# Optimization experiments

Hardware: AMD Instinct MI355X
Metric: run time of the kernel (lower is better)

The kernel has to match this reference:

```python
import jax, jax.numpy as jnp
import numpy as np

N_NODES = 50000
D = 100          # hidden_size == out_size
STEP = 1
B, N, L = 512, 64, 64
STDV = 1.0 / np.sqrt(D)


def _uniform(key, shape):
    return jax.random.uniform(key, shape, jnp.float32, -STDV, STDV)


def setup_inputs() -> dict:
    key = jax.random.key(0)
    ks = jax.random.split(key, 16)
    inp = {
        'adj_in': jax.random.uniform(ks[0], (B, N, N), jnp.float32),
        'adj_out': jax.random.uniform(ks[1], (B, N, N), jnp.float32),
        'item': jax.random.randint(ks[2], (B, N), 0, N_NODES, jnp.int32),
        'alias': jax.random.randint(ks[3], (B, L), 0, N, jnp.int32),
        'mask': jnp.ones((B, L), jnp.float32),
        'tar': jax.random.randint(ks[4], (B,), 0, N_NODES - 1, jnp.int32) + 1,
        # learned parameters
        'embedding': _uniform(ks[5], (N_NODES, D)),
        'W_in': _uniform(ks[6], (D, D)),
        'b_in': _uniform(ks[7], (D,)),
        'W_out': _uniform(ks[8], (D, D)),
        'b_out': _uniform(ks[9], (D,)),
        'gate_kernel': _uniform(ks[10], (3 * D, 2 * D)),
        'gate_bias': jnp.ones((2 * D,), jnp.float32),
        'cand_kernel': _uniform(ks[11], (3 * D, D)),
        'cand_bias': jnp.zeros((D,), jnp.float32),
        'nasr_w1': _uniform(ks[12], (D, D)),
        'nasr_w2': _uniform(ks[13], (D, D)),
        'nasr_v': _uniform(ks[14], (1, D)),
        'nasr_b': jnp.zeros((D,), jnp.float32),
    }
    return inp


def _ggnn(embedding, item, adj_in, adj_out, W_in, b_in, W_out, b_out,
          gate_kernel, gate_bias, cand_kernel, cand_bias):
    fin = embedding[item]                                 # [B, N, D]
    for _ in range(STEP):
        fi = jnp.einsum('bnd,de->bne', fin, W_in) + b_in   # [B, N, D]
        fo = jnp.einsum('bnd,de->bne', fin, W_out) + b_out
        av = jnp.concatenate([jnp.matmul(adj_in, fi), jnp.matmul(adj_out, fo)], axis=-1)  # [B, N, 2D]
        x = av.reshape(-1, 2 * D)
        h = fin.reshape(-1, D)
        # TF GRUCell math
        gates = jax.nn.sigmoid(jnp.concatenate([x, h], -1) @ gate_kernel + gate_bias)
        r, u = jnp.split(gates, 2, axis=-1)
        c = jnp.tanh(jnp.concatenate([x, r * h], -1) @ cand_kernel + cand_bias)
        fin = (u * h + (1.0 - u) * c).reshape(fin.shape)
    return fin


def _forward(adj_in, adj_out, mask, embedding, W_in, b_in, W_out, b_out,
             gate_kernel, gate_bias, cand_kernel, cand_bias,
             nasr_w1, nasr_w2, nasr_v, nasr_b, item, alias, tar):
    re = _ggnn(embedding, item, adj_in, adj_out, W_in, b_in, W_out, b_out,
               gate_kernel, gate_bias, cand_kernel, cand_bias)   # [B, N, D]
    bsz = re.shape[0]
    rm = jnp.sum(mask, axis=1).astype(jnp.int32)                 # [B]
    rows = jnp.arange(bsz)
    last_id = alias[rows, rm - 1]                                # [B]
    last_h = re[rows, last_id]                                   # [B, D]
    seq_h = jnp.take_along_axis(re, alias[..., None], axis=1)    # [B, L, D]
    last = last_h @ nasr_w1                                      # [B, D]
    seq = jnp.einsum('bld,de->ble', seq_h, nasr_w2)              # [B, L, D]
    m = jax.nn.sigmoid(last[:, None, :] + seq + nasr_b)          # [B, L, D]
    coef = (m @ nasr_v[0]) * mask                                # [B, L]
    ma = jnp.sum(coef[..., None] * seq_h, axis=1)                # [B, D]
    logits = ma @ embedding[1:].T                                # [B, n_nodes-1]
    labels = tar - 1
    logp = jax.nn.log_softmax(logits, axis=-1)
    loss = -jnp.mean(logp[rows, labels])
    return loss, logits


def reference(adj_in, adj_out, item, alias, mask, tar, embedding,
              W_in, b_in, W_out, b_out, gate_kernel, gate_bias,
              cand_kernel, cand_bias, nasr_w1, nasr_w2, nasr_v, nasr_b):
    return _forward(adj_in, adj_out, mask, embedding, W_in, b_in, W_out, b_out,
                    gate_kernel, gate_bias, cand_kernel, cand_bias,
                    nasr_w1, nasr_w2, nasr_v, nasr_b, item, alias, tar)
```

## Files before the change

### kernel.cpp

```cpp
#include <hip/hip_runtime.h>
#include <math.h>

#define BB    512
#define NNODE 64
#define LLEN  64
#define DD    100
#define NNODES 50000
#define NM1   49999
#define KP    128
#define KAV   224
#define KTOT  352
#define NCB   391
#define SHIFT 20.0f

typedef __attribute__((ext_vector_type(8))) short short8;
typedef __attribute__((ext_vector_type(4))) short short4_t;
typedef __attribute__((ext_vector_type(4))) float f32x4;
typedef unsigned short ushort_t;

__device__ __forceinline__ float sigm(float x) { return 1.0f / (1.0f + __expf(-x)); }
__device__ __forceinline__ float mytanh(float x) {
  x = fminf(15.0f, fmaxf(-15.0f, x));
  float e = __expf(-2.0f * x);
  return (1.0f - e) / (1.0f + e);
}
__device__ __forceinline__ float f4c(const float4& v, int k) { return ((const float*)&v)[k]; }
__device__ __forceinline__ ushort_t f2bf(float f) {
  union { float f; unsigned u; } v; v.f = f;
  unsigned r = v.u + 0x7FFF + ((v.u >> 16) & 1);
  return (ushort_t)(r >> 16);
}
__device__ __forceinline__ float bf2f(ushort_t s) {
  union { unsigned u; float f; } v; v.u = ((unsigned)s) << 16;
  return v.f;
}
__device__ __forceinline__ short8 cvt8(const float* __restrict__ p) {
  float4 v0 = *(const float4*)p, v1 = *(const float4*)(p + 4);
  short8 r;
  r[0] = (short)f2bf(v0.x); r[1] = (short)f2bf(v0.y);
  r[2] = (short)f2bf(v0.z); r[3] = (short)f2bf(v0.w);
  r[4] = (short)f2bf(v1.x); r[5] = (short)f2bf(v1.y);
  r[6] = (short)f2bf(v1.z); r[7] = (short)f2bf(v1.w);
  return r;
}

__global__ __launch_bounds__(256) void k_cvt_emb2(
    const float* __restrict__ emb, ushort_t* __restrict__ eb2)
{
  const int tid = blockIdx.x * 256 + threadIdx.x;
  const int r = tid >> 5, c4 = (tid & 31) * 4;
  if (r >= NNODES) return;
  short4_t o = {0, 0, 0, 0};
  if (c4 < DD) {
    float4 v = *(const float4*)(emb + (size_t)r * DD + c4);
    o.x = (short)f2bf(f4c(v, 0)); o.y = (short)f2bf(f4c(v, 1));
    o.z = (short)f2bf(f4c(v, 2)); o.w = (short)f2bf(f4c(v, 3));
  }
  *(short4_t*)(eb2 + (size_t)r * KP + c4) = o;
}

__global__ __launch_bounds__(256) void k_cvt_w(
    const float* __restrict__ Wi, const float* __restrict__ Wo,
    const float* __restrict__ gk, const float* __restrict__ ck,
    ushort_t* __restrict__ WioT, ushort_t* __restrict__ gkT,
    ushort_t* __restrict__ ckT)
{
  const int idx = blockIdx.x * 256 + threadIdx.x;
  const int y = blockIdx.y;
  if (y == 0) {
    if (idx >= 208 * 128) return;
    int n = idx >> 7, k = idx & 127;
    float v = 0.0f;
    if (k < DD) {
      if (n < 100) v = Wi[k * DD + n];
      else if (n < 200) v = Wo[k * DD + (n - 100)];
    }
    WioT[idx] = f2bf(v);
  } else if (y == 1) {
    if (idx >= 208 * KTOT) return;
    int n = idx / KTOT, k = idx - n * KTOT;
    float v = 0.0f;
    if (n < 200) {
      if (k < KAV) { if (k < 200) v = gk[k * 200 + n]; }
      else { int kk = k - KAV; if (kk < 100) v = gk[(200 + kk) * 200 + n]; }
    }
    gkT[idx] = f2bf(v);
  } else {
    if (idx >= 112 * KTOT) return;
    int n = idx / KTOT, k = idx - n * KTOT;
    float v = 0.0f;
    if (n < 100) {
      if (k < KAV) { if (k < 200) v = ck[k * DD + n]; }
      else { int kk = k - KAV; if (kk < 100) v = ck[(200 + kk) * DD + n]; }
    }
    ckT[idx] = f2bf(v);
  }
}

__global__ __launch_bounds__(256) void k_fio_av(
    const ushort_t* __restrict__ eb2, const int* __restrict__ item,
    const ushort_t* __restrict__ WioT,
    const float* __restrict__ bi, const float* __restrict__ bo,
    const float* __restrict__ adj_in, const float* __restrict__ adj_out,
    ushort_t* __restrict__ avb)
{
  __shared__ ushort_t s_f[2][112][72];
  const int t = threadIdx.x, wave = t >> 6, lane = t & 63;
  const int n16 = lane & 15, quad = lane >> 4;
  const int b = blockIdx.x;
  const int m0 = b * 64 + wave * 16;

  for (int idx = t; idx < 2 * 12 * 64; idx += 256) {
    int which = idx / 768, rem = idx - which * 768;
    s_f[which][100 + rem / 64][rem & 63] = 0;
  }

  const ushort_t* arow = eb2 + (size_t)item[m0 + n16] * KP + quad * 8;
  short8 af[4];
#pragma unroll
  for (int ks = 0; ks < 4; ++ks) af[ks] = *(const short8*)(arow + ks * 32);

  const int node0 = wave * 16 + quad * 4;
#pragma unroll
  for (int sub = 0; sub < 13; ++sub) {
    const ushort_t* brow = WioT + (size_t)(sub * 16 + n16) * KP + quad * 8;
    f32x4 acc = {0.0f, 0.0f, 0.0f, 0.0f};
#pragma unroll
    for (int ks = 0; ks < 4; ++ks)
      acc = __builtin_amdgcn_mfma_f32_16x16x32_bf16(af[ks], *(const short8*)(brow + ks * 32), acc, 0, 0, 0);
    const int col = sub * 16 + n16;
    if (col < 200) {
      const float bias = (col < 100) ? bi[col] : bo[col - 100];
      short4_t st;
#pragma unroll
      for (int r = 0; r < 4; ++r) ((ushort_t*)&st)[r] = f2bf(acc[r] + bias);
      const int which = (col < 100) ? 0 : 1;
      const int c = (col < 100) ? col : col - 100;
      *(short4_t*)&s_f[which][c][node0] = st;
    }
  }
  __syncthreads();

  const float* aI = adj_in  + ((size_t)b * 64 + wave * 16 + n16) * 64 + quad * 8;
  const float* aO = adj_out + ((size_t)b * 64 + wave * 16 + n16) * 64 + quad * 8;
  short8 afI[2], afO[2];
#pragma unroll
  for (int ks = 0; ks < 2; ++ks) {
    afI[ks] = cvt8(aI + ks * 32);
    afO[ks] = cvt8(aO + ks * 32);
  }
#pragma unroll
  for (int sub = 0; sub < 7; ++sub) {
    const int col = sub * 16 + n16;
    const ushort_t* bI = &s_f[0][col][quad * 8];
    const ushort_t* bO = &s_f[1][col][quad * 8];
    f32x4 accI = {0, 0, 0, 0}, accO = {0, 0, 0, 0};
#pragma unroll
    for (int ks = 0; ks < 2; ++ks) {
      accI = __builtin_amdgcn_mfma_f32_16x16x32_bf16(afI[ks], *(const short8*)(bI + ks * 32), accI, 0, 0, 0);
      accO = __builtin_amdgcn_mfma_f32_16x16x32_bf16(afO[ks], *(const short8*)(bO + ks * 32), accO, 0, 0, 0);
    }
    if (col < 100) {
#pragma unroll
      for (int r = 0; r < 4; ++r) {
        const size_t row = (size_t)b * 64 + wave * 16 + quad * 4 + r;
        avb[row * KAV + col] = f2bf(accI[r]);
        avb[row * KAV + 100 + col] = f2bf(accO[r]);
      }
    }
  }
}

__global__ __launch_bounds__(256) void k_gru_mfma(
    const ushort_t* __restrict__ avb, const ushort_t* __restrict__ eb2,
    const int* __restrict__ item,
    const ushort_t* __restrict__ gkT, const float* __restrict__ gb,
    const ushort_t* __restrict__ ckT, const float* __restrict__ cbs,
    float* __restrict__ fin2)
{
  __shared__ ushort_t s_h[4][16][136];
  __shared__ ushort_t s_rh[4][16][136];
  __shared__ float    s_u[4][16][104];
  const int t = threadIdx.x, wave = t >> 6, lane = t & 63;
  const int n16 = lane & 15, quad = lane >> 4;
  const int m0 = (blockIdx.x * 4 + wave) * 16;

  {
    const int row_s = lane & 15, chunk = lane >> 4;
    const ushort_t* hsrc = eb2 + (size_t)item[m0 + row_s] * KP + chunk * 32;
#pragma unroll
    for (int j = 0; j < 4; ++j)
      *(short8*)&s_h[wave][row_s][chunk * 32 + j * 8] = *(const short8*)(hsrc + j * 8);
#pragma unroll
    for (int j = 0; j < 7; ++j)
      s_rh[wave][row_s][100 + chunk * 7 + j] = 0;
  }

  const ushort_t* avrow = avb + (size_t)(m0 + n16) * KAV + quad * 8;
  short8 afa[7];
#pragma unroll
  for (int ks = 0; ks < 7; ++ks) afa[ks] = *(const short8*)(avrow + ks * 32);
  const ushort_t* hrow = eb2 + (size_t)item[m0 + n16] * KP + quad * 8;
  short8 afh[4];
#pragma unroll
  for (int ks = 0; ks < 4; ++ks) afh[ks] = *(const short8*)(hrow + ks * 32);
  __syncthreads();

#pragma unroll
  for (int sub = 0; sub < 13; ++sub) {
    const ushort_t* brow = gkT + (size_t)(sub * 16 + n16) * KTOT + quad * 8;
    f32x4 acc = {0, 0, 0, 0};
#pragma unroll
    for (int ks = 0; ks < 7; ++ks)
      acc = __builtin_amdgcn_mfma_f32_16x16x32_bf16(afa[ks], *(const short8*)(brow + ks * 32), acc, 0, 0, 0);
#pragma unroll
    for (int ks = 0; ks < 4; ++ks)
      acc = __builtin_amdgcn_mfma_f32_16x16x32_bf16(afh[ks], *(const short8*)(brow + KAV + ks * 32), acc, 0, 0, 0);
    const int col = sub * 16 + n16;
    if (col < 200) {
      const float bias = gb[col];
#pragma unroll
      for (int r = 0; r < 4; ++r) {
        const int row = quad * 4 + r;
        const float g = sigm(acc[r] + bias);
        if (col < 100) {
          s_rh[wave][row][col] = f2bf(g * bf2f(s_h[wave][row][col]));
        } else {
          s_u[wave][row][col - 100] = g;
        }
      }
    }
  }
  __syncthreads();

  short8 afr[4];
#pragma unroll
  for (int ks = 0; ks < 4; ++ks) afr[ks] = *(const short8*)&s_rh[wave][n16][ks * 32];
#pragma unroll
  for (int sub = 0; sub < 7; ++sub) {
    const ushort_t* brow = ckT + (size_t)(sub * 16 + n16) * KTOT + quad * 8;
    f32x4 acc = {0, 0, 0, 0};
#pragma unroll
    for (int ks = 0; ks < 7; ++ks)
      acc = __builtin_amdgcn_mfma_f32_16x16x32_bf16(afa[ks], *(const short8*)(brow + ks * 32), acc, 0, 0, 0);
#pragma unroll
    for (int ks = 0; ks < 4; ++ks)
      acc = __builtin_amdgcn_mfma_f32_16x16x32_bf16(afr[ks], *(const short8*)(brow + KAV + ks * 32), acc, 0, 0, 0);
    const int col = sub * 16 + n16;
    if (col < 100) {
      const float bias = cbs[col];
#pragma unroll
      for (int r = 0; r < 4; ++r) {
        const int row = quad * 4 + r;
        const float c = mytanh(acc[r] + bias);
        const float u = s_u[wave][row][col];
        const float hv = bf2f(s_h[wave][row][col]);
        fin2[(size_t)(m0 + row) * DD + col] = u * hv + (1.0f - u) * c;
      }
    }
  }
}

__global__ __launch_bounds__(256) void k_attn(
    const float* __restrict__ fin2, const int* __restrict__ alias_,
    const float* __restrict__ mask,
    const float* __restrict__ w1, const float* __restrict__ w2,
    const float* __restrict__ nv, const float* __restrict__ nb,
    ushort_t* __restrict__ mab)
{
  __shared__ float s_seqh[NNODE * DD];
  __shared__ float s_m[NNODE * DD];
  __shared__ float s_last[DD];
  __shared__ float s_coef[NNODE];
  __shared__ int s_lastid;
  const int b = blockIdx.x, t = threadIdx.x;

  if (t == 0) {
    float s = 0.0f;
    for (int l = 0; l < LLEN; ++l) s += mask[b * LLEN + l];
    int rm = (int)(s + 0.5f);
    s_lastid = alias_[b * LLEN + rm - 1];
  }
  for (int idx = t; idx < NNODE * DD; idx += 256) {
    int l = idx / DD, d = idx - l * DD;
    int n = alias_[b * LLEN + l];
    s_seqh[idx] = fin2[((size_t)b * NNODE + n) * DD + d];
  }
  __syncthreads();

  if (t < DD) {
    const float* lh = fin2 + ((size_t)b * NNODE + s_lastid) * DD;
    float acc = 0.0f;
    for (int k = 0; k < DD; ++k) acc += lh[k] * w1[k * DD + t];
    s_last[t] = acc;
  }
  __syncthreads();

  {
    const int tx = t & 31, ty = t >> 5, cb4 = tx * 4;
    if (cb4 < DD) {
      float acc[8][4] = {};
      for (int k4 = 0; k4 < 25; ++k4) {
        float4 bv[4];
#pragma unroll
        for (int kk = 0; kk < 4; ++kk) bv[kk] = *(const float4*)(w2 + (size_t)(k4 * 4 + kk) * DD + cb4);
#pragma unroll
        for (int i = 0; i < 8; ++i) {
          float4 a = *(const float4*)(&s_seqh[(ty * 8 + i) * DD + k4 * 4]);
#pragma unroll
          for (int kk = 0; kk < 4; ++kk) {
            float av_ = f4c(a, kk);
#pragma unroll
            for (int j = 0; j < 4; ++j) acc[i][j] += av_ * f4c(bv[kk], j);
          }
        }
      }
#pragma unroll
      for (int i = 0; i < 8; ++i) {
        int l = ty * 8 + i;
#pragma unroll
        for (int j = 0; j < 4; ++j) {
          int e = cb4 + j;
          s_m[l * DD + e] = sigm(acc[i][j] + s_last[e] + nb[e]);
        }
      }
    }
  }
  __syncthreads();

  if (t < LLEN) {
    float acc = 0.0f;
    for (int e = 0; e < DD; ++e) acc += s_m[t * DD + e] * nv[e];
    s_coef[t] = acc * mask[b * LLEN + t];
  }
  __syncthreads();

  if (t < DD) {
    float acc = 0.0f;
    for (int l = 0; l < LLEN; ++l) acc += s_coef[l] * s_seqh[l * DD + t];
    mab[(size_t)b * KP + t] = f2bf(acc);
  } else if (t < KP) {
    mab[(size_t)b * KP + t] = 0;
  }
}

__global__ __launch_bounds__(256) void k_logits_mfma(
    const ushort_t* __restrict__ eb2, const ushort_t* __restrict__ mab,
    float* __restrict__ out, float* __restrict__ sump)
{
  __shared__ float s_o[16][512];
  const int t = threadIdx.x;
  const int wave = t >> 6, lane = t & 63;
  const int n16 = lane & 15, quad = lane >> 4;
  const int bid = blockIdx.x;
  const int xcd = bid & 7;
  const int j = bid >> 3;
  const int grpl = j >> 5;
  const int lgmax = (xcd < 2) ? 13 : 12;
  if (grpl >= lgmax) return;
  const int stripe = j & 31;
  const int cg = ((xcd < 2) ? xcd * 13 : 26 + (xcd - 2) * 12) + grpl;
  const int m0 = stripe * 16;
  const int cblk = cg * 4 + wave;

  short8 afr[4];
  const ushort_t* abase = mab + (size_t)(m0 + n16) * KP + quad * 8;
#pragma unroll
  for (int ks = 0; ks < 4; ++ks) afr[ks] = *(const short8*)(abase + ks * 32);

  float s[4] = {0.0f, 0.0f, 0.0f, 0.0f};
  if (cblk < NCB) {
#pragma unroll
    for (int sub = 0; sub < 8; ++sub) {
      const int c = cblk * 128 + sub * 16 + n16;
      const ushort_t* bbase = eb2 + (size_t)((c < NM1) ? (c + 1) : 0) * KP + quad * 8;
      f32x4 acc = {0.0f, 0.0f, 0.0f, 0.0f};
#pragma unroll
      for (int ks = 0; ks < 4; ++ks) {
        short8 bfr = *(const short8*)(bbase + ks * 32);
        acc = __builtin_amdgcn_mfma_f32_16x16x32_bf16(afr[ks], bfr, acc, 0, 0, 0);
      }
#pragma unroll
      for (int r = 0; r < 4; ++r) {
        s_o[quad * 4 + r][wave * 128 + sub * 16 + n16] = acc[r];
        if (c < NM1) s[r] += __expf(acc[r] - SHIFT);
      }
    }
  }
  __syncthreads();

  float* lgp = out + 1;
  const int half = t >> 7, tc = t & 127;
#pragma unroll
  for (int it = 0; it < 8; ++it) {
    const int row = it * 2 + half;
    const size_t gr = m0 + row;
    f32x4 v = *(const f32x4*)&s_o[row][tc * 4];
    const int c0 = cg * 512 + tc * 4;
    if (c0 + 3 < NM1) {
      __builtin_nontemporal_store(v, (f32x4*)(lgp + gr * NM1 + c0));
    } else {
#pragma unroll
      for (int e = 0; e < 4; ++e)
        if (c0 + e < NM1)
          __builtin_nontemporal_store(v[e], lgp + gr * NM1 + c0 + e);
    }
  }

  if (cblk < NCB) {
    const int row0 = m0 + quad * 4;
#pragma unroll
    for (int r = 0; r < 4; ++r) {
      float x = s[r];
      x += __shfl_xor(x, 1, 64);
      x += __shfl_xor(x, 2, 64);
      x += __shfl_xor(x, 4, 64);
      x += __shfl_xor(x, 8, 64);
      if (n16 == 0) sump[(size_t)(row0 + r) * NCB + cblk] = x;
    }
  }
}

__global__ __launch_bounds__(64) void k_lse(
    const float* __restrict__ sump, const float* __restrict__ out,
    const int* __restrict__ tar, float* __restrict__ rowterm)
{
  const int r = blockIdx.x, t = threadIdx.x;
  float s = 0.0f;
  for (int i = t; i < NCB; i += 64) s += sump[(size_t)r * NCB + i];
  for (int m = 1; m < 64; m <<= 1) s += __shfl_xor(s, m, 64);
  if (t == 0) {
    int label = tar[r] - 1;
    const float* lg = out + 1;
    rowterm[r] = lg[(size_t)r * NM1 + label] - (logf(s) + SHIFT);
  }
}

__global__ __launch_bounds__(256) void k_loss(
    const float* __restrict__ rowterm, float* __restrict__ out)
{
  const int t = threadIdx.x;
  __shared__ float red[4];
  float s = rowterm[t] + rowterm[t + 256];
  for (int m = 1; m < 64; m <<= 1) s += __shfl_xor(s, m, 64);
  if ((t & 63) == 0) red[t >> 6] = s;
  __syncthreads();
  if (t == 0) out[0] = -(red[0] + red[1] + red[2] + red[3]) / (float)BB;
}

extern "C" void kernel_launch(void* const* d_in, const int* in_sizes, int n_in,
                              void* d_out, int out_size, void* d_ws, size_t ws_size,
                              hipStream_t stream)
{
  (void)in_sizes; (void)n_in; (void)out_size; (void)ws_size;
  const float* adj_in  = (const float*)d_in[0];
  const float* adj_out = (const float*)d_in[1];
  const int*   item    = (const int*)d_in[2];
  const int*   alias_  = (const int*)d_in[3];
  const float* mask    = (const float*)d_in[4];
  const int*   tar     = (const int*)d_in[5];
  const float* emb     = (const float*)d_in[6];
  const float* W_in    = (const float*)d_in[7];
  const float* b_in    = (const float*)d_in[8];
  const float* W_out   = (const float*)d_in[9];
  const float* b_out   = (const float*)d_in[10];
  const float* gk      = (const float*)d_in[11];
  const float* gb      = (const float*)d_in[12];
  const float* ck      = (const float*)d_in[13];
  const float* cbs     = (const float*)d_in[14];
  const float* w1      = (const float*)d_in[15];
  const float* w2      = (const float*)d_in[16];
  const float* nv      = (const float*)d_in[17];
  const float* nb      = (const float*)d_in[18];
  float* out = (float*)d_out;

  ushort_t* usw = (ushort_t*)d_ws;
  ushort_t* eb2  = usw;
  ushort_t* avb  = usw + 6400000;
  ushort_t* WioT = usw + 13740032;
  ushort_t* gkT  = usw + 13766656;
  ushort_t* ckT  = usw + 13839872;
  ushort_t* mab  = usw + 13879296;
  float* fpool   = (float*)(usw + 13944832);
  float* fin2    = fpool;
  float* sump    = fpool + 3276800;
  float* rowterm = fpool + 3276800 + 200192;

  k_cvt_emb2<<<dim3(6250), 256, 0, stream>>>(emb, eb2);
  k_cvt_w   <<<dim3(287, 3), 256, 0, stream>>>(W_in, W_out, gk, ck, WioT, gkT, ckT);
  k_fio_av  <<<dim3(512), 256, 0, stream>>>(eb2, item, WioT, b_in, b_out, adj_in, adj_out, avb);
  k_gru_mfma<<<dim3(512), 256, 0, stream>>>(avb, eb2, item, gkT, gb, ckT, cbs, fin2);
  k_attn    <<<dim3(512), 256, 0, stream>>>(fin2, alias_, mask, w1, w2, nv, nb, mab);
  k_logits_mfma<<<dim3(3328), 256, 0, stream>>>(eb2, mab, out, sump);
  k_lse     <<<dim3(512), 64, 0, stream>>>(sump, out, tar, rowterm);
  k_loss    <<<dim3(1), 256, 0, stream>>>(rowterm, out);
}
```

Baseline: 301.4 us.

## Fuse GGNN, GRU and attention into one per-batch kernel; merge launches

Merges the embedding and weight conversion kernels into one launch and fuses the adjacency propagation, GRU cell and attention stages into a single 512-thread kernel per batch. Intermediate av and fin tensors now stay in shared memory instead of going through global memory, and the loss reduction is folded into the LSE kernel with an atomicAdd. This cuts global round-trips and launch count, but uses about 107KB of shared memory per block, which limits occupancy. Atomic float accumulation also makes the loss summation order nondeterministic.

```diff
diff --git a/kernel.cpp b/kernel.cpp
--- a/kernel.cpp
+++ b/kernel.cpp
@@ -44,29 +44,32 @@
   return r;
 }
 
-__global__ __launch_bounds__(256) void k_cvt_emb2(
-    const float* __restrict__ emb, ushort_t* __restrict__ eb2)
-{
-  const int tid = blockIdx.x * 256 + threadIdx.x;
-  const int r = tid >> 5, c4 = (tid & 31) * 4;
-  if (r >= NNODES) return;
-  short4_t o = {0, 0, 0, 0};
-  if (c4 < DD) {
-    float4 v = *(const float4*)(emb + (size_t)r * DD + c4);
-    o.x = (short)f2bf(f4c(v, 0)); o.y = (short)f2bf(f4c(v, 1));
-    o.z = (short)f2bf(f4c(v, 2)); o.w = (short)f2bf(f4c(v, 3));
-  }
-  *(short4_t*)(eb2 + (size_t)r * KP + c4) = o;
-}
-
-__global__ __launch_bounds__(256) void k_cvt_w(
+__global__ __launch_bounds__(256) void k_cvt_all(
+    const float* __restrict__ emb,
     const float* __restrict__ Wi, const float* __restrict__ Wo,
     const float* __restrict__ gk, const float* __restrict__ ck,
-    ushort_t* __restrict__ WioT, ushort_t* __restrict__ gkT,
-    ushort_t* __restrict__ ckT)
+    ushort_t* __restrict__ eb2, ushort_t* __restrict__ WioT,
+    ushort_t* __restrict__ gkT, ushort_t* __restrict__ ckT,
+    float* __restrict__ out)
 {
-  const int idx = blockIdx.x * 256 + threadIdx.x;
-  const int y = blockIdx.y;
+  const int bid = blockIdx.x, t = threadIdx.x;
+  if (bid == 0 && t == 0) out[0] = 0.0f;
+  if (bid < 6250) {
+    const int tid = bid * 256 + t;
+    const int r = tid >> 5, c4 = (tid & 31) * 4;
+    if (r >= NNODES) return;
+    short4_t o = {0, 0, 0, 0};
+    if (c4 < DD) {
+      float4 v = *(const float4*)(emb + (size_t)r * DD + c4);
+      o.x = (short)f2bf(f4c(v, 0)); o.y = (short)f2bf(f4c(v, 1));
+      o.z = (short)f2bf(f4c(v, 2)); o.w = (short)f2bf(f4c(v, 3));
+    }
+    *(short4_t*)(eb2 + (size_t)r * KP + c4) = o;
+    return;
+  }
+  const int rem = bid - 6250;
+  const int y = rem / 287;
+  const int idx = (rem - y * 287) * 256 + t;
   if (y == 0) {
     if (idx >= 208 * 128) return;
     int n = idx >> 7, k = idx & 127;
@@ -97,200 +100,188 @@
   }
 }
 
-__global__ __launch_bounds__(256) void k_fio_av(
+__global__ __launch_bounds__(512) void k_fused(
     const ushort_t* __restrict__ eb2, const int* __restrict__ item,
     const ushort_t* __restrict__ WioT,
     const float* __restrict__ bi, const float* __restrict__ bo,
     const float* __restrict__ adj_in, const float* __restrict__ adj_out,
-    ushort_t* __restrict__ avb)
-{
-  __shared__ ushort_t s_f[2][112][72];
-  const int t = threadIdx.x, wave = t >> 6, lane = t & 63;
-  const int n16 = lane & 15, quad = lane >> 4;
-  const int b = blockIdx.x;
-  const int m0 = b * 64 + wave * 16;
-
-  for (int idx = t; idx < 2 * 12 * 64; idx += 256) {
-    int which = idx / 768, rem = idx - which * 768;
-    s_f[which][100 + rem / 64][rem & 63] = 0;
-  }
-
-  const ushort_t* arow = eb2 + (size_t)item[m0 + n16] * KP + quad * 8;
-  short8 af[4];
-#pragma unroll
-  for (int ks = 0; ks < 4; ++ks) af[ks] = *(const short8*)(arow + ks * 32);
-
-  const int node0 = wave * 16 + quad * 4;
-#pragma unroll
-  for (int sub = 0; sub < 13; ++sub) {
-    const ushort_t* brow = WioT + (size_t)(sub * 16 + n16) * KP + quad * 8;
-    f32x4 acc = {0.0f, 0.0f, 0.0f, 0.0f};
-#pragma unroll
-    for (int ks = 0; ks < 4; ++ks)
-      acc = __builtin_amdgcn_mfma_f32_16x16x32_bf16(af[ks], *(const short8*)(brow + ks * 32), acc, 0, 0, 0);
-    const int col = sub * 16 + n16;
-    if (col < 200) {
-      const float bias = (col < 100) ? bi[col] : bo[col - 100];
-      short4_t st;
-#pragma unroll
-      for (int r = 0; r < 4; ++r) ((ushort_t*)&st)[r] = f2bf(acc[r] + bias);
-      const int which = (col < 100) ? 0 : 1;
-      const int c = (col < 100) ? col : col - 100;
-      *(short4_t*)&s_f[which][c][node0] = st;
-    }
-  }
-  __syncthreads();
-
-  const float* aI = adj_in  + ((size_t)b * 64 + wave * 16 + n16) * 64 + quad * 8;
-  const float* aO = adj_out + ((size_t)b * 64 + wave * 16 + n16) * 64 + quad * 8;
-  short8 afI[2], afO[2];
-#pragma unroll
-  for (int ks = 0; ks < 2; ++ks) {
-    afI[ks] = cvt8(aI + ks * 32);
-    afO[ks] = cvt8(aO + ks * 32);
-  }
-#pragma unroll
-  for (int sub = 0; sub < 7; ++sub) {
-    const int col = sub * 16 + n16;
-    const ushort_t* bI = &s_f[0][col][quad * 8];
-    const ushort_t* bO = &s_f[1][col][quad * 8];
-    f32x4 accI = {0, 0, 0, 0}, accO = {0, 0, 0, 0};
-#pragma unroll
-    for (int ks = 0; ks < 2; ++ks) {
-      accI = __builtin_amdgcn_mfma_f32_16x16x32_bf16(afI[ks], *(const short8*)(bI + ks * 32), accI, 0, 0, 0);
-      accO = __builtin_amdgcn_mfma_f32_16x16x32_bf16(afO[ks], *(const short8*)(bO + ks * 32), accO, 0, 0, 0);
-    }
-    if (col < 100) {
-#pragma unroll
-      for (int r = 0; r < 4; ++r) {
-        const size_t row = (size_t)b * 64 + wave * 16 + quad * 4 + r;
-        avb[row * KAV + col] = f2bf(accI[r]);
-        avb[row * KAV + 100 + col] = f2bf(accO[r]);
-      }
-    }
-  }
-}
-
-__global__ __launch_bounds__(256) void k_gru_mfma(
-    const ushort_t* __restrict__ avb, const ushort_t* __restrict__ eb2,
-    const int* __restrict__ item,
     const ushort_t* __restrict__ gkT, const float* __restrict__ gb,
     const ushort_t* __restrict__ ckT, const float* __restrict__ cbs,
-    float* __restrict__ fin2)
-{
-  __shared__ ushort_t s_h[4][16][136];
-  __shared__ ushort_t s_rh[4][16][136];
-  __shared__ float    s_u[4][16][104];
-  const int t = threadIdx.x, wave = t >> 6, lane = t & 63;
-  const int n16 = lane & 15, quad = lane >> 4;
-  const int m0 = (blockIdx.x * 4 + wave) * 16;
-
-  {
-    const int row_s = lane & 15, chunk = lane >> 4;
-    const ushort_t* hsrc = eb2 + (size_t)item[m0 + row_s] * KP + chunk * 32;
-#pragma unroll
-    for (int j = 0; j < 4; ++j)
-      *(short8*)&s_h[wave][row_s][chunk * 32 + j * 8] = *(const short8*)(hsrc + j * 8);
-#pragma unroll
-    for (int j = 0; j < 7; ++j)
-      s_rh[wave][row_s][100 + chunk * 7 + j] = 0;
-  }
-
-  const ushort_t* avrow = avb + (size_t)(m0 + n16) * KAV + quad * 8;
-  short8 afa[7];
-#pragma unroll
-  for (int ks = 0; ks < 7; ++ks) afa[ks] = *(const short8*)(avrow + ks * 32);
-  const ushort_t* hrow = eb2 + (size_t)item[m0 + n16] * KP + quad * 8;
-  short8 afh[4];
-#pragma unroll
-  for (int ks = 0; ks < 4; ++ks) afh[ks] = *(const short8*)(hrow + ks * 32);
-  __syncthreads();
-
-#pragma unroll
-  for (int sub = 0; sub < 13; ++sub) {
-    const ushort_t* brow = gkT + (size_t)(sub * 16 + n16) * KTOT + quad * 8;
-    f32x4 acc = {0, 0, 0, 0};
-#pragma unroll
-    for (int ks = 0; ks < 7; ++ks)
-      acc = __builtin_amdgcn_mfma_f32_16x16x32_bf16(afa[ks], *(const short8*)(brow + ks * 32), acc, 0, 0, 0);
-#pragma unroll
-    for (int ks = 0; ks < 4; ++ks)
-      acc = __builtin_amdgcn_mfma_f32_16x16x32_bf16(afh[ks], *(const short8*)(brow + KAV + ks * 32), acc, 0, 0, 0);
-    const int col = sub * 16 + n16;
-    if (col < 200) {
-      const float bias = gb[col];
-#pragma unroll
-      for (int r = 0; r < 4; ++r) {
-        const int row = quad * 4 + r;
-        const float g = sigm(acc[r] + bias);
-        if (col < 100) {
-          s_rh[wave][row][col] = f2bf(g * bf2f(s_h[wave][row][col]));
-        } else {
-          s_u[wave][row][col - 100] = g;
-        }
-      }
-    }
-  }
-  __syncthreads();
-
-  short8 afr[4];
-#pragma unroll
-  for (int ks = 0; ks < 4; ++ks) afr[ks] = *(const short8*)&s_rh[wave][n16][ks * 32];
-#pragma unroll
-  for (int sub = 0; sub < 7; ++sub) {
-    const ushort_t* brow = ckT + (size_t)(sub * 16 + n16) * KTOT + quad * 8;
-    f32x4 acc = {0, 0, 0, 0};
-#pragma unroll
-    for (int ks = 0; ks < 7; ++ks)
-      acc = __builtin_amdgcn_mfma_f32_16x16x32_bf16(afa[ks], *(const short8*)(brow + ks * 32), acc, 0, 0, 0);
-#pragma unroll
-    for (int ks = 0; ks < 4; ++ks)
-      acc = __builtin_amdgcn_mfma_f32_16x16x32_bf16(afr[ks], *(const short8*)(brow + KAV + ks * 32), acc, 0, 0, 0);
-    const int col = sub * 16 + n16;
-    if (col < 100) {
-      const float bias = cbs[col];
-#pragma unroll
-      for (int r = 0; r < 4; ++r) {
-        const int row = quad * 4 + r;
-        const float c = mytanh(acc[r] + bias);
-        const float u = s_u[wave][row][col];
-        const float hv = bf2f(s_h[wave][row][col]);
-        fin2[(size_t)(m0 + row) * DD + col] = u * hv + (1.0f - u) * c;
-      }
-    }
-  }
-}
-
-__global__ __launch_bounds__(256) void k_attn(
-    const float* __restrict__ fin2, const int* __restrict__ alias_,
-    const float* __restrict__ mask,
+    const int* __restrict__ alias_, const float* __restrict__ mask,
     const float* __restrict__ w1, const float* __restrict__ w2,
     const float* __restrict__ nv, const float* __restrict__ nb,
     ushort_t* __restrict__ mab)
 {
-  __shared__ float s_seqh[NNODE * DD];
-  __shared__ float s_m[NNODE * DD];
-  __shared__ float s_last[DD];
-  __shared__ float s_coef[NNODE];
-  __shared__ int s_lastid;
-  const int b = blockIdx.x, t = threadIdx.x;
-
-  if (t == 0) {
-    float s = 0.0f;
-    for (int l = 0; l < LLEN; ++l) s += mask[b * LLEN + l];
-    int rm = (int)(s + 0.5f);
-    s_lastid = alias_[b * LLEN + rm - 1];
-  }
-  for (int idx = t; idx < NNODE * DD; idx += 256) {
-    int l = idx / DD, d = idx - l * DD;
-    int n = alias_[b * LLEN + l];
-    s_seqh[idx] = fin2[((size_t)b * NNODE + n) * DD + d];
+  __shared__ __align__(16) char pool[106928];
+  ushort_t (*s_f)[112][72] = (ushort_t (*)[112][72])(pool);
+  ushort_t (*s_rh)[136]    = (ushort_t (*)[136])(pool);
+  float    (*s_m)[104]     = (float (*)[104])(pool);
+  ushort_t (*s_av)[232]    = (ushort_t (*)[232])(pool + 32256);
+  float    (*s_fin)[104]   = (float (*)[104])(pool + 32256);
+  ushort_t (*s_h)[136]     = (ushort_t (*)[136])(pool + 61952);
+  float    (*s_u)[104]     = (float (*)[104])(pool + 79360);
+  float* s_last   = (float*)(pool + 105984);
+  float* s_coef   = (float*)(pool + 106400);
+  int*   s_idx    = (int*)(pool + 106656);
+  int*   s_lastid = (int*)(pool + 106912);
+
+  const int t = threadIdx.x;
+  const int w8 = t >> 6, lane = t & 63;
+  const int rw = w8 & 3, ch = w8 >> 2;
+  const int n16 = lane & 15, quad = lane >> 4;
+  const int b = blockIdx.x;
+
+  {
+    const int row = t >> 3, seg = t & 7;
+    const ushort_t* hsrc = eb2 + (size_t)item[b * 64 + row] * KP + seg * 16;
+    *(short8*)&s_h[row][seg * 16]     = *(const short8*)(hsrc);
+    *(short8*)&s_h[row][seg * 16 + 8] = *(const short8*)(hsrc + 8);
+  }
+  if (t >= 64 && t < 128) {
+    const int r2 = t - 64;
+#pragma unroll
+    for (int c = 200; c < 224; ++c) s_av[r2][c] = 0;
+  }
+  for (int idx = t; idx < 2 * 12 * 64; idx += 512) {
+    int which = idx / 768, rem = idx - which * 768;
+    s_f[which][100 + rem / 64][rem & 63] = 0;
+  }
+  __syncthreads();
+
+  short8 af[4];
+#pragma unroll
+  for (int ks = 0; ks < 4; ++ks)
+    af[ks] = *(const short8*)&s_h[rw * 16 + n16][quad * 8 + ks * 32];
+
+  {
+    const int node0 = rw * 16 + quad * 4;
+    const int s0 = ch ? 7 : 0, s1 = ch ? 13 : 7;
+    for (int sub = s0; sub < s1; ++sub) {
+      const ushort_t* brow = WioT + (size_t)(sub * 16 + n16) * KP + quad * 8;
+      f32x4 acc = {0.0f, 0.0f, 0.0f, 0.0f};
+#pragma unroll
+      for (int ks = 0; ks < 4; ++ks)
+        acc = __builtin_amdgcn_mfma_f32_16x16x32_bf16(af[ks], *(const short8*)(brow + ks * 32), acc, 0, 0, 0);
+      const int col = sub * 16 + n16;
+      if (col < 200) {
+        const float bias = (col < 100) ? bi[col] : bo[col - 100];
+        short4_t st;
+#pragma unroll
+        for (int r = 0; r < 4; ++r) ((ushort_t*)&st)[r] = f2bf(acc[r] + bias);
+        const int which = (col < 100) ? 0 : 1;
+        const int c = (col < 100) ? col : col - 100;
+        *(short4_t*)&s_f[which][c][node0] = st;
+      }
+    }
+  }
+  __syncthreads();
+
+  {
+    const float* aX = (ch ? adj_out : adj_in)
+                      + ((size_t)b * 64 + rw * 16 + n16) * 64 + quad * 8;
+    short8 afX[2];
+    afX[0] = cvt8(aX); afX[1] = cvt8(aX + 32);
+    for (int sub = 0; sub < 7; ++sub) {
+      const int col = sub * 16 + n16;
+      const ushort_t* bX = &s_f[ch][col][quad * 8];
+      f32x4 acc = {0.0f, 0.0f, 0.0f, 0.0f};
+#pragma unroll
+      for (int ks = 0; ks < 2; ++ks)
+        acc = __builtin_amdgcn_mfma_f32_16x16x32_bf16(afX[ks], *(const short8*)(bX + ks * 32), acc, 0, 0, 0);
+      if (col < 100) {
+#pragma unroll
+        for (int r = 0; r < 4; ++r)
+          s_av[rw * 16 + quad * 4 + r][ch * 100 + col] = f2bf(acc[r]);
+      }
+    }
+  }
+  __syncthreads();
+
+  if (t < 64) {
+#pragma unroll
+    for (int c = 100; c < 128; ++c) s_rh[t][c] = 0;
+  }
+  short8 afa[7];
+#pragma unroll
+  for (int ks = 0; ks < 7; ++ks)
+    afa[ks] = *(const short8*)&s_av[rw * 16 + n16][quad * 8 + ks * 32];
+
+  {
+    const int s0 = ch ? 7 : 0, s1 = ch ? 13 : 7;
+    for (int sub = s0; sub < s1; ++sub) {
+      const ushort_t* brow = gkT + (size_t)(sub * 16 + n16) * KTOT + quad * 8;
+      f32x4 acc = {0.0f, 0.0f, 0.0f, 0.0f};
+#pragma unroll
+      for (int ks = 0; ks < 7; ++ks)
+        acc = __builtin_amdgcn_mfma_f32_16x16x32_bf16(afa[ks], *(const short8*)(brow + ks * 32), acc, 0, 0, 0);
+#pragma unroll
+      for (int ks = 0; ks < 4; ++ks)
+        acc = __builtin_amdgcn_mfma_f32_16x16x32_bf16(af[ks], *(const short8*)(brow + KAV + ks * 32), acc, 0, 0, 0);
+      const int col = sub * 16 + n16;
+      if (col < 200) {
+        const float bias = gb[col];
+#pragma unroll
+        for (int r = 0; r < 4; ++r) {
+          const int row = rw * 16 + quad * 4 + r;
+          const float g = sigm(acc[r] + bias);
+          if (col < 100) s_rh[row][col] = f2bf(g * bf2f(s_h[row][col]));
+          else           s_u[row][col - 100] = g;
+        }
+      }
+    }
+  }
+  __syncthreads();
+
+  short8 afr[4];
+#pragma unroll
+  for (int ks = 0; ks < 4; ++ks)
+    afr[ks] = *(const short8*)&s_rh[rw * 16 + n16][quad * 8 + ks * 32];
+
+  {
+    const int s0 = ch ? 4 : 0, s1 = ch ? 7 : 4;
+    for (int sub = s0; sub < s1; ++sub) {
+      const ushort_t* brow = ckT + (size_t)(sub * 16 + n16) * KTOT + quad * 8;
+      f32x4 acc = {0.0f, 0.0f, 0.0f, 0.0f};
+#pragma unroll
+      for (int ks = 0; ks < 7; ++ks)
+        acc = __builtin_amdgcn_mfma_f32_16x16x32_bf16(afa[ks], *(const short8*)(brow + ks * 32), acc, 0, 0, 0);
+#pragma unroll
+      for (int ks = 0; ks < 4; ++ks)
+        acc = __builtin_amdgcn_mfma_f32_16x16x32_bf16(afr[ks], *(const short8*)(brow + KAV + ks * 32), acc, 0, 0, 0);
+      const int col = sub * 16 + n16;
+      if (col < 100) {
+        const float bias = cbs[col];
+#pragma unroll
+        for (int r = 0; r < 4; ++r) {
+          const int row = rw * 16 + quad * 4 + r;
+          const float c_ = mytanh(acc[r] + bias);
+          const float u = s_u[row][col];
+          const float hv = bf2f(s_h[row][col]);
+          s_fin[row][col] = u * hv + (1.0f - u) * c_;
+        }
+      }
+    }
+  }
+  __syncthreads();
+
+  if (t < 64) {
+    float v = mask[b * LLEN + t];
+    v += __shfl_xor(v, 1, 64);  v += __shfl_xor(v, 2, 64);
+    v += __shfl_xor(v, 4, 64);  v += __shfl_xor(v, 8, 64);
+    v += __shfl_xor(v, 16, 64); v += __shfl_xor(v, 32, 64);
+    if (t == 0) {
+      int rm = (int)(v + 0.5f);
+      *s_lastid = alias_[b * LLEN + rm - 1];
+    }
+  } else if (t < 128) {
+    s_idx[t - 64] = alias_[b * LLEN + (t - 64)];
   }
   __syncthreads();
 
   if (t < DD) {
-    const float* lh = fin2 + ((size_t)b * NNODE + s_lastid) * DD;
+    const float* lh = s_fin[*s_lastid];
     float acc = 0.0f;
+#pragma unroll 4
     for (int k = 0; k < DD; ++k) acc += lh[k] * w1[k * DD + t];
     s_last[t] = acc;
   }
@@ -299,14 +290,17 @@
   {
     const int tx = t & 31, ty = t >> 5, cb4 = tx * 4;
     if (cb4 < DD) {
-      float acc[8][4] = {};
+      float acc[4][4] = {};
+      const float* frs[4] = { s_fin[s_idx[ty * 4 + 0]], s_fin[s_idx[ty * 4 + 1]],
+                              s_fin[s_idx[ty * 4 + 2]], s_fin[s_idx[ty * 4 + 3]] };
       for (int k4 = 0; k4 < 25; ++k4) {
         float4 bv[4];
 #pragma unroll
-        for (int kk = 0; kk < 4; ++kk) bv[kk] = *(const float4*)(w2 + (size_t)(k4 * 4 + kk) * DD + cb4);
-#pragma unroll
-        for (int i = 0; i < 8; ++i) {
-          float4 a = *(const float4*)(&s_seqh[(ty * 8 + i) * DD + k4 * 4]);
+        for (int kk = 0; kk < 4; ++kk)
+          bv[kk] = *(const float4*)(w2 + (size_t)(k4 * 4 + kk) * DD + cb4);
+#pragma unroll
+        for (int i = 0; i < 4; ++i) {
+          float4 a = *(const float4*)(frs[i] + k4 * 4);
 #pragma unroll
           for (int kk = 0; kk < 4; ++kk) {
             float av_ = f4c(a, kk);
@@ -316,12 +310,12 @@
         }
       }
 #pragma unroll
-      for (int i = 0; i < 8; ++i) {
-        int l = ty * 8 + i;
+      for (int i = 0; i < 4; ++i) {
+        const int l = ty * 4 + i;
 #pragma unroll
         for (int j = 0; j < 4; ++j) {
-          int e = cb4 + j;
-          s_m[l * DD + e] = sigm(acc[i][j] + s_last[e] + nb[e]);
+          const int e = cb4 + j;
+          s_m[l][e] = sigm(acc[i][j] + s_last[e] + nb[e]);
         }
       }
     }
@@ -330,14 +324,16 @@
 
   if (t < LLEN) {
     float acc = 0.0f;
-    for (int e = 0; e < DD; ++e) acc += s_m[t * DD + e] * nv[e];
+#pragma unroll 4
+    for (int e = 0; e < DD; ++e) acc += s_m[t][e] * nv[e];
     s_coef[t] = acc * mask[b * LLEN + t];
   }
   __syncthreads();
 
   if (t < DD) {
     float acc = 0.0f;
-    for (int l = 0; l < LLEN; ++l) acc += s_coef[l] * s_seqh[l * DD + t];
+#pragma unroll 4
+    for (int l = 0; l < LLEN; ++l) acc += s_coef[l] * s_fin[s_idx[l]][t];
     mab[(size_t)b * KP + t] = f2bf(acc);
   } else if (t < KP) {
     mab[(size_t)b * KP + t] = 0;
@@ -421,9 +417,9 @@
   }
 }
 
-__global__ __launch_bounds__(64) void k_lse(
-    const float* __restrict__ sump, const float* __restrict__ out,
-    const int* __restrict__ tar, float* __restrict__ rowterm)
+__global__ __launch_bounds__(64) void k_lse_loss(
+    const float* __restrict__ sump, float* __restrict__ out,
+    const int* __restrict__ tar)
 {
   const int r = blockIdx.x, t = threadIdx.x;
   float s = 0.0f;
@@ -432,20 +428,9 @@
   if (t == 0) {
     int label = tar[r] - 1;
     const float* lg = out + 1;
-    rowterm[r] = lg[(size_t)r * NM1 + label] - (logf(s) + SHIFT);
-  }
-}
-
-__global__ __launch_bounds__(256) void k_loss(
-    const float* __restrict__ rowterm, float* __restrict__ out)
-{
-  const int t = threadIdx.x;
-  __shared__ float red[4];
-  float s = rowterm[t] + rowterm[t + 256];
-  for (int m = 1; m < 64; m <<= 1) s += __shfl_xor(s, m, 64);
-  if ((t & 63) == 0) red[t >> 6] = s;
-  __syncthreads();
-  if (t == 0) out[0] = -(red[0] + red[1] + red[2] + red[3]) / (float)BB;
+    float rt = lg[(size_t)r * NM1 + label] - (logf(s) + SHIFT);
+    atomicAdd(out, -rt / (float)BB);
+  }
 }
 
 extern "C" void kernel_launch(void* const* d_in, const int* in_sizes, int n_in,
@@ -476,22 +461,18 @@
 
   ushort_t* usw = (ushort_t*)d_ws;
   ushort_t* eb2  = usw;
-  ushort_t* avb  = usw + 6400000;
   ushort_t* WioT = usw + 13740032;
   ushort_t* gkT  = usw + 13766656;
   ushort_t* ckT  = usw + 13839872;
   ushort_t* mab  = usw + 13879296;
   float* fpool   = (float*)(usw + 13944832);
-  float* fin2    = fpool;
   float* sump    = fpool + 3276800;
-  float* rowterm = fpool + 3276800 + 200192;
-
-  k_cvt_emb2<<<dim3(6250), 256, 0, stream>>>(emb, eb2);
-  k_cvt_w   <<<dim3(287, 3), 256, 0, stream>>>(W_in, W_out, gk, ck, WioT, gkT, ckT);
-  k_fio_av  <<<dim3(512), 256, 0, stream>>>(eb2, item, WioT, b_in, b_out, adj_in, adj_out, avb);
-  k_gru_mfma<<<dim3(512), 256, 0, stream>>>(avb, eb2, item, gkT, gb, ckT, cbs, fin2);
-  k_attn    <<<dim3(512), 256, 0, stream>>>(fin2, alias_, mask, w1, w2, nv, nb, mab);
+
+  k_cvt_all <<<dim3(7111), 256, 0, stream>>>(emb, W_in, W_out, gk, ck,
+                                             eb2, WioT, gkT, ckT, out);
+  k_fused   <<<dim3(512), 512, 0, stream>>>(eb2, item, WioT, b_in, b_out,
+                                            adj_in, adj_out, gkT, gb, ckT, cbs,
+                                            alias_, mask, w1, w2, nv, nb, mab);
   k_logits_mfma<<<dim3(3328), 256, 0, stream>>>(eb2, mab, out, sump);
-  k_lse     <<<dim3(512), 64, 0, stream>>>(sump, out, tar, rowterm);
-  k_loss    <<<dim3(1), 256, 0, stream>>>(rowterm, out);
-}
+  k_lse_loss<<<dim3(512), 64, 0, stream>>>(sump, out, tar);
+}
```

Result: slower. 326.8 us (+8.4%).
